# Kernel optimization log

Hardware: AMD Instinct MI355X
Metric: run time of the kernel (lower is better)

Reference implementation:

```python
import jax, jax.numpy as jnp
import numpy as np

N_UP, N_DN = 64, 64
L = 10.0
BATCH = 8192


def _create_centers(N_up, N_dn, L):
    n = 1
    while n ** 3 < max(N_up, N_dn):
        n += 1
    a = L / n
    coords = np.linspace(0.0, L - a, n)
    grid = np.stack(np.meshgrid(coords, coords, coords, indexing='ij'), axis=-1).reshape(-1, 3)
    centers_up = grid[:N_up]
    centers_dn = (grid + a / 2.0)[:N_dn]
    return jnp.asarray(centers_up, jnp.float32), jnp.asarray(centers_dn, jnp.float32)


def _slater_logdet(rs_spin, centers, alpha):
    # rs_spin: [B, N, 3], centers: [M, 3] -> Phi: [B, N, M]
    dr = rs_spin[:, :, None, :] - centers[None, None, :, :]
    dr_p = (L / jnp.pi) * jnp.sin(jnp.pi * dr / L)  # smooth periodic displacement
    r2 = jnp.sum(dr_p * dr_p, axis=-1)
    Phi = jnp.exp(-alpha * r2)
    _, logdet = jnp.linalg.slogdet(Phi)
    return logdet  # [B]


def setup_inputs() -> dict:
    key = jax.random.key(0)
    k1, _ = jax.random.split(key)
    rs = jax.random.uniform(k1, (BATCH, N_UP + N_DN, 3), dtype=jnp.float32) * L
    log_alpha = jnp.asarray(np.log(np.sqrt(100.0) / L ** 2), dtype=jnp.float32)
    return {"rs": rs, "log_alpha": log_alpha}


def reference(rs, log_alpha):
    centers_up, centers_dn = _create_centers(N_UP, N_DN, L)
    alpha = jnp.exp(log_alpha)
    alpha = jnp.clip(alpha, 0.5 / L ** 2, 200.0 / L ** 2)
    log_up = _slater_logdet(rs[:, :N_UP], centers_up, alpha)
    log_dn = _slater_logdet(rs[:, N_UP:N_UP + N_DN], centers_dn, alpha)
    return log_up + log_dn  # [B]
```

## Files before the change

### kernel.cpp

```cpp
#include <hip/hip_runtime.h>

__device__ __forceinline__ float rdlane(float v, int l) {
    return __int_as_float(__builtin_amdgcn_readlane(__float_as_int(v), l));
}

template <int CTRL>
__device__ __forceinline__ float dpp_max_step(float x) {
    int t = __builtin_amdgcn_update_dpp(0, __float_as_int(x), CTRL, 0xF, 0xF, true);
    return fmaxf(x, __int_as_float(t));
}

__device__ __forceinline__ float wave_max_to_lane63(float x) {
    x = dpp_max_step<0xB1>(x);
    x = dpp_max_step<0x4E>(x);
    x = dpp_max_step<0x141>(x);
    x = dpp_max_step<0x140>(x);
    x = dpp_max_step<0x142>(x);
    x = dpp_max_step<0x143>(x);
    return x;
}

__global__ __launch_bounds__(128, 2) void slater_logdet_kernel(
        const float* __restrict__ rs, const float* __restrict__ log_alpha_p,
        float* __restrict__ out) {
    const int b    = blockIdx.x;
    const int tid  = threadIdx.x;
    const int wave = tid >> 6;
    const int lane = tid & 63;

    const float Lbox = 10.0f;
    const float PI_F = 3.14159265358979323846f;

    float alpha = __expf(log_alpha_p[0]);
    alpha = fminf(fmaxf(alpha, 0.5f / (Lbox * Lbox)), 200.0f / (Lbox * Lbox));

    const float* rp = rs + (size_t)b * 384 + (size_t)(wave * 64 + lane) * 3;
    float x = rp[0], y = rp[1], z = rp[2];

    float sx, cx, sy, cy, sz, cz;
    __sincosf(x * (PI_F / Lbox), &sx, &cx);
    __sincosf(y * (PI_F / Lbox), &sy, &cy);
    __sincosf(z * (PI_F / Lbox), &sz, &cz);

    const float off = wave ? 0.5f : 0.0f;
    const float LPI = Lbox / PI_F;
    float ex[4], ey[4], ez[4];
#pragma unroll
    for (int m = 0; m < 4; ++m) {
        float sp, cp;
        __sincosf((PI_F * 0.25f) * ((float)m + off), &sp, &cp);
        float dx = LPI * (sx * cp - cx * sp);
        float dy = LPI * (sy * cp - cy * sp);
        float dz = LPI * (sz * cp - cz * sp);
        ex[m] = __expf(-alpha * dx * dx);
        ey[m] = __expf(-alpha * dy * dy);
        ez[m] = __expf(-alpha * dz * dz);
    }
    float exy[16];
#pragma unroll
    for (int q = 0; q < 16; ++q) exy[q] = ex[q >> 2] * ey[q & 3];
    float A[64];
#pragma unroll
    for (int j = 0; j < 64; ++j) A[j] = exy[j >> 2] * ez[j & 3];

    float flag   = 0.0f;
    float logdet = 0.0f;
    const int lane_v = lane;
#pragma unroll
    for (int k = 0; k < 64; ++k) {
        float key  = fabsf(A[k]) + flag;
        float gmax = rdlane(wave_max_to_lane63(key), 63);
        unsigned long long ball = __ballot(key == gmax);
        int p = (int)(__ffsll(ball) - 1);

        float pv  = rdlane(A[k], p);
        float inv = __builtin_amdgcn_rcpf(pv);
        inv = inv * (2.0f - pv * inv);
        logdet += __logf(fabsf(pv));

        flag = (lane_v == p) ? -__builtin_huge_valf() : flag;

        float m = A[k] * inv;
#pragma unroll
        for (int j = k + 1; j < 64; ++j) {
            float s = rdlane(A[j], p);
            A[j] = __builtin_fmaf(-m, s, A[j]);
        }
    }

    __shared__ float partial[2];
    if (lane == 0) partial[wave] = logdet;
    __syncthreads();
    if (tid == 0) out[b] = partial[0] + partial[1];
}

extern "C" void kernel_launch(void* const* d_in, const int* in_sizes, int n_in,
                              void* d_out, int out_size, void* d_ws, size_t ws_size,
                              hipStream_t stream) {
    const float* rs = (const float*)d_in[0];
    const float* la = (const float*)d_in[1];
    float* out      = (float*)d_out;
    slater_logdet_kernel<<<out_size, 128, 0, stream>>>(rs, la, out);
}
```

Baseline: 305.1 us.

## Split each 64x64 LU across two waves with interleaved columns and LDS broadcast

Each matrix's columns are now split between two waves by parity, so a block runs four waves instead of two and each wave holds 32 columns. At each step the wave owning the pivot column finds the pivot, computes the multipliers and publishes them through LDS. Both waves then apply the rank-1 update to their own columns. This halves per-wave register pressure and serial update work. In exchange it adds a __syncthreads and LDS traffic at every one of the 64 steps, and the non-owning wave idles while the pivot is searched.

```diff
diff --git a/kernel.cpp b/kernel.cpp
--- a/kernel.cpp
+++ b/kernel.cpp
@@ -20,29 +20,67 @@
     return x;
 }
 
-__global__ __launch_bounds__(128, 2) void slater_logdet_kernel(
-        const float* __restrict__ rs, const float* __restrict__ log_alpha_p,
-        float* __restrict__ out) {
-    const int b    = blockIdx.x;
-    const int tid  = threadIdx.x;
-    const int wave = tid >> 6;
-    const int lane = tid & 63;
+struct Shared {
+    float m[2][2][64];
+    int   p[2][2];
+    float partial[2][2];
+};
 
+template <int K, int W>
+struct LUStep {
+    __device__ __forceinline__ static void run(float (&A)[32], float& flag,
+            float& logdet, int lane, int mat, Shared* sh) {
+        constexpr int OP = K & 1;
+        constexpr int kk = K >> 1;
+        float mcoef;
+        int p_s;
+        if constexpr (W == OP) {
+            float key  = fabsf(A[kk]) + flag;
+            float gmax = rdlane(wave_max_to_lane63(key), 63);
+            unsigned long long ball = __ballot(key == gmax);
+            p_s = (int)(__ffsll(ball) - 1);
+            float pv  = rdlane(A[kk], p_s);
+            float inv = __builtin_amdgcn_rcpf(pv);
+            inv = inv * (2.0f - pv * inv);
+            logdet += __logf(fabsf(pv));
+            mcoef = A[kk] * inv;
+            sh->m[mat][OP][lane] = mcoef;
+            if (lane == 0) sh->p[mat][OP] = p_s;
+        }
+        __syncthreads();
+        if constexpr (W != OP) {
+            int pv_ = sh->p[mat][OP];
+            p_s    = __builtin_amdgcn_readfirstlane(pv_);
+            mcoef  = sh->m[mat][OP][lane];
+        }
+        flag = (lane == p_s) ? -__builtin_huge_valf() : flag;
+        constexpr int JLO = (K + 2 - W) >> 1;
+#pragma unroll
+        for (int jj = JLO; jj < 32; ++jj) {
+            float s = rdlane(A[jj], p_s);
+            A[jj] = __builtin_fmaf(-mcoef, s, A[jj]);
+        }
+        LUStep<K + 1, W>::run(A, flag, logdet, lane, mat, sh);
+    }
+};
+template <int W>
+struct LUStep<64, W> {
+    __device__ __forceinline__ static void run(float (&)[32], float&, float&,
+                                               int, int, Shared*) {}
+};
+
+template <int W>
+__device__ __forceinline__ void run_half(const float* rp, float alpha, float off,
+                                         int lane, int mat, Shared* sh,
+                                         float* out, int b, int tid) {
     const float Lbox = 10.0f;
     const float PI_F = 3.14159265358979323846f;
-
-    float alpha = __expf(log_alpha_p[0]);
-    alpha = fminf(fmaxf(alpha, 0.5f / (Lbox * Lbox)), 200.0f / (Lbox * Lbox));
-
-    const float* rp = rs + (size_t)b * 384 + (size_t)(wave * 64 + lane) * 3;
     float x = rp[0], y = rp[1], z = rp[2];
-
     float sx, cx, sy, cy, sz, cz;
     __sincosf(x * (PI_F / Lbox), &sx, &cx);
     __sincosf(y * (PI_F / Lbox), &sy, &cy);
     __sincosf(z * (PI_F / Lbox), &sz, &cz);
 
-    const float off = wave ? 0.5f : 0.0f;
     const float LPI = Lbox / PI_F;
     float ex[4], ey[4], ez[4];
 #pragma unroll
@@ -59,39 +97,47 @@
     float exy[16];
 #pragma unroll
     for (int q = 0; q < 16; ++q) exy[q] = ex[q >> 2] * ey[q & 3];
-    float A[64];
+    float A[32];
 #pragma unroll
-    for (int j = 0; j < 64; ++j) A[j] = exy[j >> 2] * ez[j & 3];
-
-    float flag   = 0.0f;
-    float logdet = 0.0f;
-    const int lane_v = lane;
-#pragma unroll
-    for (int k = 0; k < 64; ++k) {
-        float key  = fabsf(A[k]) + flag;
-        float gmax = rdlane(wave_max_to_lane63(key), 63);
-        unsigned long long ball = __ballot(key == gmax);
-        int p = (int)(__ffsll(ball) - 1);
-
-        float pv  = rdlane(A[k], p);
-        float inv = __builtin_amdgcn_rcpf(pv);
-        inv = inv * (2.0f - pv * inv);
-        logdet += __logf(fabsf(pv));
-
-        flag = (lane_v == p) ? -__builtin_huge_valf() : flag;
-
-        float m = A[k] * inv;
-#pragma unroll
-        for (int j = k + 1; j < 64; ++j) {
-            float s = rdlane(A[j], p);
-            A[j] = __builtin_fmaf(-m, s, A[j]);
-        }
+    for (int jj = 0; jj < 32; ++jj) {
+        constexpr int W_ = W;
+        int j = 2 * jj + W_;
+        A[jj] = exy[j >> 2] * ez[j & 3];
     }
 
-    __shared__ float partial[2];
-    if (lane == 0) partial[wave] = logdet;
+    float flag = 0.0f, logdet = 0.0f;
+    LUStep<0, W>::run(A, flag, logdet, lane, mat, sh);
+
+    if (lane == 0) sh->partial[mat][W] = logdet;
     __syncthreads();
-    if (tid == 0) out[b] = partial[0] + partial[1];
+    if (tid == 0)
+        out[b] = sh->partial[0][0] + sh->partial[0][1] +
+                 sh->partial[1][0] + sh->partial[1][1];
+}
+
+__global__ __launch_bounds__(256, 4) void slater_logdet_kernel(
+        const float* __restrict__ rs, const float* __restrict__ log_alpha_p,
+        float* __restrict__ out) {
+    const int b    = blockIdx.x;
+    const int tid  = threadIdx.x;
+    const int wv   = tid >> 6;
+    const int mat  = wv >> 1;
+    const int wpar = wv & 1;
+    const int lane = tid & 63;
+
+    __shared__ Shared sh;
+
+    const float Lbox = 10.0f;
+    float alpha = __expf(log_alpha_p[0]);
+    alpha = fminf(fmaxf(alpha, 0.5f / (Lbox * Lbox)), 200.0f / (Lbox * Lbox));
+
+    const float* rp = rs + (size_t)b * 384 + (size_t)(mat * 64 + lane) * 3;
+    const float off = mat ? 0.5f : 0.0f;
+
+    if (wpar == 0)
+        run_half<0>(rp, alpha, off, lane, mat, &sh, out, b, tid);
+    else
+        run_half<1>(rp, alpha, off, lane, mat, &sh, out, b, tid);
 }
 
 extern "C" void kernel_launch(void* const* d_in, const int* in_sizes, int n_in,
@@ -100,5 +146,5 @@
     const float* rs = (const float*)d_in[0];
     const float* la = (const float*)d_in[1];
     float* out      = (float*)d_out;
-    slater_logdet_kernel<<<out_size, 128, 0, stream>>>(rs, la, out);
+    slater_logdet_kernel<<<out_size, 256, 0, stream>>>(rs, la, out);
 }
```

After: 328.6 us. +7.7%, slower.
